# Kernel tuning notes

Measured on AMD Instinct MI355X. Metric: run time of the kernel, lower is better.

## Reference

```python
import jax, jax.numpy as jnp
import numpy as np

D_STATE = 16
D_CONV = 4


def silu(x):
    return x * jax.nn.sigmoid(x)


def selective_scan(x, dt, A, Bm, Cm, Dp):
    # x, dt: (B,L,P); A: (P,N); Bm, Cm: (B,L,N); Dp: (P,)
    dA = jnp.exp(dt[..., None] * A)                    # (B,L,P,N)
    dBx = (dt * x)[..., None] * Bm[:, :, None, :]      # (B,L,P,N)

    def comb(c1, c2):
        a1, b1 = c1
        a2, b2 = c2
        return a1 * a2, a2 * b1 + b2

    _, h = jax.lax.associative_scan(comb, (dA, dBx), axis=1)
    y = jnp.einsum('blpn,bln->blp', h, Cm) + x * Dp
    return y


def mamba(seq, W_in, conv_w, conv_b, W_x, W_dt, b_dt, A_log, Dp, W_out):
    # seq: (B, L, D_model)
    xz = seq @ W_in.T                                  # (B,L,2P)
    P = xz.shape[-1] // 2
    x, z = xz[..., :P], xz[..., P:]
    # causal depthwise conv over L
    xc = jnp.transpose(x, (0, 2, 1))                   # (B,P,L)
    xc = jax.lax.conv_general_dilated(xc, conv_w[:, None, :], (1,),
                                      [(D_CONV - 1, 0)], feature_group_count=P)
    x = silu(jnp.transpose(xc, (0, 2, 1)) + conv_b)    # (B,L,P)
    proj = x @ W_x.T                                   # (B,L, dt_rank+2N)
    dtr = W_dt.shape[1]
    dt = jax.nn.softplus(proj[..., :dtr] @ W_dt.T + b_dt)
    Bm = proj[..., dtr:dtr + D_STATE]
    Cm = proj[..., dtr + D_STATE:]
    A = -jnp.exp(A_log)
    y = selective_scan(x, dt, A, Bm, Cm, Dp)
    y = y * silu(z)
    return y @ W_out.T                                 # (B,L,D_model)


def oss_forward(x1, x2, W_in, conv_w, conv_b, W_x, W_dt, b_dt, A_log, Dp, W_out):
    B, C, H, W = x1.shape
    L = H * W
    seq_h = jnp.transpose(x1.reshape(B, C, L), (0, 2, 1))                       # (B, H*W, C) row-major
    seq_w = jnp.transpose(jnp.transpose(x1, (0, 1, 3, 2)).reshape(B, C, L), (0, 2, 1))  # column-major

    def run(i, s):
        return mamba(s, W_in[i], conv_w[i], conv_b[i], W_x[i], W_dt[i],
                     b_dt[i], A_log[i], Dp[i], W_out[i])

    y_hf = run(0, seq_h)
    y_hb = jnp.flip(run(1, jnp.flip(seq_h, 1)), 1)
    y_wf = run(2, seq_w)
    y_wb = jnp.flip(run(3, jnp.flip(seq_w, 1)), 1)

    y_h = jnp.transpose((y_hf + y_hb).reshape(B, H, W, C), (0, 3, 1, 2))        # (B,C,H,W)
    y_w = jnp.transpose((y_wf + y_wb).reshape(B, W, H, C), (0, 3, 2, 1))        # (B,C,H,W)
    return y_h + y_w + x2


def setup_inputs() -> dict:
    key = jax.random.key(0)
    ks = jax.random.split(key, 12)
    B, C, H, W = 2, 96, 64, 64
    P = 2 * C            # d_inner = expand * d_model = 192
    N = D_STATE
    dtr = -(-C // 16)    # dt_rank = ceil(C/16) = 6
    s = 0.02
    inp = {
        'x1': jax.random.normal(ks[0], (B, C, H, W), jnp.float32),
        'x2': jax.random.normal(ks[1], (B, C, H, W), jnp.float32),
        'W_in': jax.random.normal(ks[2], (4, 2 * P, C), jnp.float32) * s,
        'conv_w': jax.random.normal(ks[3], (4, P, D_CONV), jnp.float32) * s,
        'conv_b': jnp.zeros((4, P), jnp.float32),
        'W_x': jax.random.normal(ks[4], (4, dtr + 2 * N, P), jnp.float32) * s,
        'W_dt': jax.random.normal(ks[5], (4, P, dtr), jnp.float32) * s,
        'b_dt': jax.random.normal(ks[6], (4, P), jnp.float32) * s,
        'A_log': jnp.log(jnp.tile(jnp.arange(1.0, N + 1.0, dtype=jnp.float32), (4, P, 1))),
        'Dp': jnp.ones((4, P), jnp.float32),
        'W_out': jax.random.normal(ks[7], (4, C, P), jnp.float32) * s,
    }
    return inp


def reference(x1, x2, W_in, conv_w, conv_b, W_x, W_dt, b_dt, A_log, Dp, W_out):
    return oss_forward(x1, x2, W_in, conv_w, conv_b, W_x, W_dt, b_dt, A_log, Dp, W_out)
```

## Files before the change

kernel.cpp:

```cpp
#include <hip/hip_runtime.h>

#define D_DIRS 4
#define BB 2
#define CC 96
#define LL 4096
#define PP 192
#define TWOP 384
#define NN 16
#define DTR 6
#define NPROJ 38
#define PROJW 40
#define NCH 256
#define CLEN 16
#define SEQT 24576
#define LOG2E 1.44269504088896340736f

typedef __bf16 bf16x8 __attribute__((ext_vector_type(8)));
typedef float f32x4 __attribute__((ext_vector_type(4)));

__device__ __forceinline__ float fast_softplus(float v) {
    return fmaxf(v, 0.0f) + __logf(1.0f + __expf(-fabsf(v)));
}

__device__ __forceinline__ const float* uptr(const float* p) {
    unsigned long v = (unsigned long)p;
    unsigned lo = __builtin_amdgcn_readfirstlane((unsigned)v);
    unsigned hi = __builtin_amdgcn_readfirstlane((unsigned)(v >> 32));
    return (const float*)(((unsigned long)hi << 32) | (unsigned long)lo);
}

__device__ __constant__ float LOGN[16] = {
    0.0f, 0.6931471806f, 1.0986122887f, 1.3862943611f,
    1.6094379124f, 1.7917594692f, 1.9459101091f, 2.0794415417f,
    2.1972245773f, 2.3025850930f, 2.3978952728f, 2.4849066498f,
    2.5649493575f, 2.6390573296f, 2.7080502011f, 2.7725887222f };

#define POWERS(e1, E)                                                    \
    float E##2 = (e1)*(e1), E##4 = E##2*E##2, E##8 = E##4*E##4;          \
    float E##3 = E##2*(e1), E##5 = E##4*(e1), E##6 = E##4*E##2,          \
          E##7 = E##4*E##3, E##9 = E##8*(e1), E##10 = E##8*E##2,         \
          E##11 = E##8*E##3, E##12 = E##8*E##4, E##13 = E##8*E##5,       \
          E##14 = E##8*E##6, E##15 = E##8*E##7, E##16 = E##8*E##8;

__global__ __launch_bounds__(256) void k_setup(
    const float* __restrict__ W_in, const float* __restrict__ W_x,
    const float* __restrict__ W_out, const float* __restrict__ x1,
    __bf16* __restrict__ wbin, __bf16* __restrict__ wbx, __bf16* __restrict__ wbout,
    __bf16* __restrict__ imgH, __bf16* __restrict__ imgW)
{
    __shared__ float t[96 * 65];
    const int tid = threadIdx.x;
    if (blockIdx.x < 1074) {
        int i = blockIdx.x * 256 + tid;
        const int n0 = 4 * 384 * 104, n1 = 4 * 48 * 200, n2 = 4 * 96 * 200;
        if (i < n0) {
            int c = i % 104, jd = i / 104;
            wbin[i] = (c < 96) ? (__bf16)W_in[jd * 96 + c] : (__bf16)0.0f;
        } else if (i < n0 + n1) {
            int k = i - n0;
            int c = k % 200, jd = k / 200;
            int d = jd / 48, j = jd - d * 48;
            float v = (j < 38 && c < 192) ? W_x[(d * 38 + j) * 192 + c] : 0.0f;
            wbx[k] = (__bf16)v;
        } else if (i < n0 + n1 + n2) {
            int k = i - n0 - n1;
            int c = k % 200, jd = k / 200;
            float v = (c < 192) ? W_out[jd * 192 + c] : 0.0f;
            wbout[k] = (__bf16)v;
        }
    } else {
        const int bx = blockIdx.x - 1074;
        const int b = bx >> 6;
        const int lt = bx & 63;
        for (int i = tid; i < 96 * 64; i += 256) {
            int c = i >> 6, lw = i & 63;
            t[c * 65 + lw] = x1[((b * 96 + c) << 12) + (lt << 6) + lw];
        }
        __syncthreads();
        for (int i = tid; i < 64 * 12; i += 256) {
            int lw = i / 12, q = i - lw * 12;
            union { __bf16 h[8]; uint4 u; } pk;
#pragma unroll
            for (int j = 0; j < 8; ++j) pk.h[j] = (__bf16)t[(q * 8 + j) * 65 + lw];
            ((uint4*)(imgH + (long)((b << 12) + (lt << 6) + lw) * 104))[q] = pk.u;
            ((uint4*)(imgW + (long)((b << 12) + (lw << 6) + lt) * 104))[q] = pk.u;
        }
    }
}

__global__ __launch_bounds__(256) void k_gemm_in(
    const __bf16* __restrict__ imgH, const __bf16* __restrict__ imgW,
    const __bf16* __restrict__ wbin, __bf16* __restrict__ xzb, __bf16* __restrict__ zb)
{
    __shared__ __align__(16) __bf16 As[64 * 104];
    __shared__ __align__(16) __bf16 Bs[128 * 104];
    const int db = blockIdx.y;
    const int d = db >> 1, b = db & 1;
    const int t0 = blockIdx.x * 64;
    const int tid = threadIdx.x;
    const __bf16* img = (d < 2 ? imgH : imgW) + (long)b * (LL * 104);

    {
        uint4* adst = (uint4*)As;
        for (int i = tid; i < 832; i += 256) {
            int r = i / 13, q = i - r * 13;
            int l = (d & 1) ? (LL - 1 - (t0 + r)) : (t0 + r);
            adst[i] = ((const uint4*)(img + (long)l * 104))[q];
        }
    }

    const int lane = tid & 63;
    const int w = tid >> 6;
    const int wm = (w >> 1) * 32, wn = (w & 1) * 32;
    const int lr = lane & 15, lk = (lane >> 4) * 8;
    const int orow = (lane >> 4) * 4;

    for (int jo = 0; jo < TWOP; jo += 128) {
        __syncthreads();
        {
            const uint4* bsrc = (const uint4*)(wbin + (long)(d * TWOP + jo) * 104);
            uint4* bdst = (uint4*)Bs;
            for (int i = tid; i < 1664; i += 256) bdst[i] = bsrc[i];
        }
        __syncthreads();

#pragma unroll
        for (int half = 0; half < 2; ++half) {
            const int j0 = jo + half * 64;
            const __bf16* Bh = Bs + half * (64 * 104);
            f32x4 acc[2][2] = {{{0.f,0.f,0.f,0.f},{0.f,0.f,0.f,0.f}},
                               {{0.f,0.f,0.f,0.f},{0.f,0.f,0.f,0.f}}};
#pragma unroll
            for (int ks = 0; ks < 96; ks += 32) {
                bf16x8 a0 = *(const bf16x8*)&As[(wm + lr) * 104 + ks + lk];
                bf16x8 a1 = *(const bf16x8*)&As[(wm + 16 + lr) * 104 + ks + lk];
                bf16x8 b0 = *(const bf16x8*)&Bh[(wn + lr) * 104 + ks + lk];
                bf16x8 b1 = *(const bf16x8*)&Bh[(wn + 16 + lr) * 104 + ks + lk];
                acc[0][0] = __builtin_amdgcn_mfma_f32_16x16x32_bf16(a0, b0, acc[0][0], 0, 0, 0);
                acc[0][1] = __builtin_amdgcn_mfma_f32_16x16x32_bf16(a0, b1, acc[0][1], 0, 0, 0);
                acc[1][0] = __builtin_amdgcn_mfma_f32_16x16x32_bf16(a1, b0, acc[1][0], 0, 0, 0);
                acc[1][1] = __builtin_amdgcn_mfma_f32_16x16x32_bf16(a1, b1, acc[1][1], 0, 0, 0);
            }
#pragma unroll
            for (int mi = 0; mi < 2; ++mi)
#pragma unroll
                for (int ni = 0; ni < 2; ++ni) {
                    long mbase = (long)(db * LL + t0 + wm + mi * 16 + orow);
                    int jcol = j0 + wn + ni * 16 + lr;
                    if (j0 < PP) {
#pragma unroll
                        for (int r = 0; r < 4; ++r) xzb[(mbase + r) * PP + jcol] = (__bf16)acc[mi][ni][r];
                    } else {
#pragma unroll
                        for (int r = 0; r < 4; ++r) zb[(mbase + r) * PP + jcol - PP] = (__bf16)acc[mi][ni][r];
                    }
                }
        }
    }
}

__global__ __launch_bounds__(256) void k_convproj(
    const __bf16* __restrict__ xzb, const float* __restrict__ conv_w,
    const float* __restrict__ conv_b, const __bf16* __restrict__ wbx,
    __bf16* __restrict__ xb16, float* __restrict__ proj)
{
    __shared__ __align__(16) __bf16 As[64 * 200];
    __shared__ __align__(16) __bf16 Bs[48 * 200];
    const int db = blockIdx.y;
    const int d = db >> 1;
    const int t0 = blockIdx.x * 64;
    const int m0 = db * LL + t0;
    const int tid = threadIdx.x;

    if (tid < 192) {
        const int p = tid;
        const float* wp = conv_w + (d * PP + p) * 4;
        float w0 = wp[0], w1 = wp[1], w2 = wp[2], w3 = wp[3];
        float bias = conv_b[d * PP + p];
        const __bf16* xcol = xzb + (long)m0 * PP + p;
        float x0, x1, x2;
        if (t0 == 0) { x0 = 0.f; x1 = 0.f; x2 = 0.f; }
        else { x0 = (float)xcol[-3 * PP]; x1 = (float)xcol[-2 * PP]; x2 = (float)xcol[-PP]; }
#pragma unroll 8
        for (int t = 0; t < 64; ++t) {
            float x3 = (float)xcol[t * PP];
            float acc = bias + w0 * x0 + w1 * x1 + w2 * x2 + w3 * x3;
            float s = acc / (1.0f + __expf(-acc));
            __bf16 sb = (__bf16)s;
            As[t * 200 + p] = sb;
            xb16[(long)(m0 + t) * 200 + p] = sb;
            x0 = x1; x1 = x2; x2 = x3;
        }
    } else {
        const uint4* bsrc = (const uint4*)(wbx + (long)d * 48 * 200);
        uint4* bdst = (uint4*)Bs;
        for (int i = tid - 192; i < 1200; i += 64) bdst[i] = bsrc[i];
    }
    __syncthreads();

    const int lane = tid & 63;
    const int w = tid >> 6;
    const int lr = lane & 15, lk = (lane >> 4) * 8;
    const int orow = (lane >> 4) * 4;

    f32x4 acc[3] = {{0.f,0.f,0.f,0.f},{0.f,0.f,0.f,0.f},{0.f,0.f,0.f,0.f}};
#pragma unroll
    for (int ks = 0; ks < 192; ks += 32) {
        bf16x8 a = *(const bf16x8*)&As[(w * 16 + lr) * 200 + ks + lk];
#pragma unroll
        for (int ni = 0; ni < 3; ++ni) {
            bf16x8 bfr = *(const bf16x8*)&Bs[(ni * 16 + lr) * 200 + ks + lk];
            acc[ni] = __builtin_amdgcn_mfma_f32_16x16x32_bf16(a, bfr, acc[ni], 0, 0, 0);
        }
    }
#pragma unroll
    for (int ni = 0; ni < 3; ++ni) {
        int j = ni * 16 + lr;
        if (j < NPROJ) {
            int col = (j < 6) ? j : j + 2;
#pragma unroll
            for (int r = 0; r < 4; ++r) {
                int m = m0 + w * 16 + orow + r;
                proj[(long)m * PROJW + col] = acc[ni][r];
            }
        }
    }
}

__global__ __launch_bounds__(256) void k_gemm_out(
    const __bf16* __restrict__ ysb, const __bf16* __restrict__ wbout, float* __restrict__ yo)
{
    __shared__ __align__(16) __bf16 As[64 * 200];
    __shared__ __align__(16) __bf16 Bs[96 * 200];
    const int m0 = blockIdx.x * 64;
    const int d = m0 >> 13;
    const int tid = threadIdx.x;

    for (int i = tid; i < 1600; i += 256) {
        int r = i / 25, q = i - r * 25;
        ((uint4*)As)[i] = ((const uint4*)(ysb + (long)(m0 + r) * 200))[q];
    }
    {
        const uint4* bsrc = (const uint4*)(wbout + (long)d * 96 * 200);
        uint4* bdst = (uint4*)Bs;
        for (int i = tid; i < 2400; i += 256) bdst[i] = bsrc[i];
    }
    __syncthreads();

    const int lane = tid & 63;
    const int w = tid >> 6;
    const int wm = (w >> 1) * 32, wn = (w & 1) * 48;
    const int lr = lane & 15, lk = (lane >> 4) * 8;
    const int orow = (lane >> 4) * 4;

    f32x4 acc[2][3] = {};
#pragma unroll
    for (int ks = 0; ks < 192; ks += 32) {
        bf16x8 a0 = *(const bf16x8*)&As[(wm + lr) * 200 + ks + lk];
        bf16x8 a1 = *(const bf16x8*)&As[(wm + 16 + lr) * 200 + ks + lk];
#pragma unroll
        for (int ni = 0; ni < 3; ++ni) {
            bf16x8 bfr = *(const bf16x8*)&Bs[(wn + ni * 16 + lr) * 200 + ks + lk];
            acc[0][ni] = __builtin_amdgcn_mfma_f32_16x16x32_bf16(a0, bfr, acc[0][ni], 0, 0, 0);
            acc[1][ni] = __builtin_amdgcn_mfma_f32_16x16x32_bf16(a1, bfr, acc[1][ni], 0, 0, 0);
        }
    }
#pragma unroll
    for (int mi = 0; mi < 2; ++mi)
#pragma unroll
        for (int ni = 0; ni < 3; ++ni) {
#pragma unroll
            for (int r = 0; r < 4; ++r) {
                int m = m0 + wm + mi * 16 + orow + r;
                yo[(long)m * CC + wn + ni * 16 + lr] = acc[mi][ni][r];
            }
        }
}

__global__ __launch_bounds__(192) void k_pass1(
    const __bf16* __restrict__ xb16, const float* __restrict__ proj,
    const float* __restrict__ A_log, const float* __restrict__ W_dt,
    const float* __restrict__ b_dt,
    float* __restrict__ sdt_buf, float* __restrict__ cb_pa, float* __restrict__ cb_h)
{
    const int p = threadIdx.x;
    const int chunk = blockIdx.x;
    const int db = blockIdx.y;
    const int d = db >> 1;
    const int m0 = db * LL + chunk * CLEN;

    bool fastA = true;
    float A2[16];
    {
        const float* al = A_log + (d * PP + p) * NN;
#pragma unroll
        for (int n = 0; n < 16; ++n) {
            float av = al[n];
            fastA = fastA && (fabsf(av - LOGN[n]) < 1e-4f);
            A2[n] = av;
        }
    }
    float w[6];
    const float* wd = W_dt + (d * PP + p) * DTR;
#pragma unroll
    for (int r = 0; r < 6; ++r) w[r] = wd[r];
    const float bdt = b_dt[d * PP + p];
    float h[16];
#pragma unroll
    for (int n = 0; n < 16; ++n) h[n] = 0.f;
    float sdt = 0.f;

    const float* prow = uptr(proj + (long)m0 * PROJW);
    const __bf16* xrow = xb16 + (long)m0 * 200 + p;

    if (fastA) {
#pragma unroll
        for (int s = 0; s < CLEN; ++s) {
            const float* row = prow + s * PROJW;
            float4 d0 = *(const float4*)(row);
            float4 d1 = *(const float4*)(row + 4);
            float v = bdt + d0.x*w[0] + d0.y*w[1] + d0.z*w[2] + d0.w*w[3] + d1.x*w[4] + d1.y*w[5];
            float dtv = fast_softplus(v);
            sdt += dtv;
            float dtx = dtv * (float)xrow[s * 200];
            float e1 = exp2f(-LOG2E * dtv);
            POWERS(e1, e)
            const float4* B4 = (const float4*)(row + 8);
            float4 B0 = B4[0], B1 = B4[1], B2v = B4[2], B3 = B4[3];
            h[0]  = e1 *h[0]  + dtx*B0.x;  h[1]  = e2 *h[1]  + dtx*B0.y;
            h[2]  = e3 *h[2]  + dtx*B0.z;  h[3]  = e4 *h[3]  + dtx*B0.w;
            h[4]  = e5 *h[4]  + dtx*B1.x;  h[5]  = e6 *h[5]  + dtx*B1.y;
            h[6]  = e7 *h[6]  + dtx*B1.z;  h[7]  = e8 *h[7]  + dtx*B1.w;
            h[8]  = e9 *h[8]  + dtx*B2v.x; h[9]  = e10*h[9]  + dtx*B2v.y;
            h[10] = e11*h[10] + dtx*B2v.z; h[11] = e12*h[11] + dtx*B2v.w;
            h[12] = e13*h[12] + dtx*B3.x;  h[13] = e14*h[13] + dtx*B3.y;
            h[14] = e15*h[14] + dtx*B3.z;  h[15] = e16*h[15] + dtx*B3.w;
        }
        const long cbase = (long)chunk * SEQT + db * PP + p;
        sdt_buf[chunk * 1536 + db * PP + p] = sdt;
#pragma unroll
        for (int n = 0; n < 16; ++n) cb_h[cbase + n * 1536] = h[n];
    } else {
#pragma unroll
        for (int n = 0; n < 16; ++n) A2[n] = -__expf(A2[n]) * LOG2E;
        for (int s = 0; s < CLEN; ++s) {
            const float* row = prow + s * PROJW;
            float4 d0 = *(const float4*)(row);
            float4 d1 = *(const float4*)(row + 4);
            float v = bdt + d0.x*w[0] + d0.y*w[1] + d0.z*w[2] + d0.w*w[3] + d1.x*w[4] + d1.y*w[5];
            float dtv = fast_softplus(v);
            sdt += dtv;
            float dtx = dtv * (float)xrow[s * 200];
            const float* B = row + 8;
#pragma unroll
            for (int n = 0; n < 16; ++n)
                h[n] = exp2f(dtv * A2[n]) * h[n] + dtx * B[n];
        }
        const long cbase = (long)chunk * SEQT + db * PP + p;
#pragma unroll
        for (int n = 0; n < 16; ++n) {
            cb_pa[cbase + n * 1536] = exp2f(A2[n] * sdt);
            cb_h [cbase + n * 1536] = h[n];
        }
    }
}

__global__ void k_chunkscan(const float* __restrict__ A_log, const float* __restrict__ sdt,
                            const float* __restrict__ cb_pa, float* __restrict__ cb_h)
{
    int j = blockIdx.x * 256 + threadIdx.x;
    int n = j / 1536;
    int r = j - n * 1536;
    int d = r / 384;
    int p = r % PP;

    bool fastA = true;
    const float* al = A_log + (d * PP + p) * NN;
#pragma unroll
    for (int k = 0; k < 16; ++k) fastA = fastA && (fabsf(al[k] - LOGN[k]) < 1e-4f);

    float run = 0.0f;
    if (fastA) {
        const float scale = -LOG2E * (float)(n + 1);
        for (int c = 0; c < NCH; c += 8) {
            float sv[8], hh[8];
#pragma unroll
            for (int i = 0; i < 8; ++i) {
                sv[i] = sdt[(c + i) * 1536 + r];
                hh[i] = cb_h[(long)(c + i) * SEQT + j];
            }
#pragma unroll
            for (int i = 0; i < 8; ++i) {
                cb_h[(long)(c + i) * SEQT + j] = run;
                run = exp2f(scale * sv[i]) * run + hh[i];
            }
        }
    } else {
        for (int c = 0; c < NCH; c += 8) {
            float pa[8], hh[8];
#pragma unroll
            for (int i = 0; i < 8; ++i) {
                long o = (long)(c + i) * SEQT + j;
                pa[i] = cb_pa[o]; hh[i] = cb_h[o];
            }
#pragma unroll
            for (int i = 0; i < 8; ++i) {
                cb_h[(long)(c + i) * SEQT + j] = run;
                run = pa[i] * run + hh[i];
            }
        }
    }
}

__global__ __launch_bounds__(192) void k_pass2(
    const __bf16* __restrict__ xb16, const float* __restrict__ proj,
    const float* __restrict__ A_log, const float* __restrict__ W_dt,
    const float* __restrict__ b_dt, const float* __restrict__ Dp,
    const __bf16* __restrict__ zb, const float* __restrict__ cb_h,
    __bf16* __restrict__ ysb)
{
    const int p = threadIdx.x;
    const int chunk = blockIdx.x;
    const int db = blockIdx.y;
    const int d = db >> 1;
    const int m0 = db * LL + chunk * CLEN;

    bool fastA = true;
    float A2[16];
    {
        const float* al = A_log + (d * PP + p) * NN;
#pragma unroll
        for (int n = 0; n < 16; ++n) {
            float av = al[n];
            fastA = fastA && (fabsf(av - LOGN[n]) < 1e-4f);
            A2[n] = av;
        }
    }
    float w[6];
    const float* wd = W_dt + (d * PP + p) * DTR;
#pragma unroll
    for (int r = 0; r < 6; ++r) w[r] = wd[r];
    const float bdt = b_dt[d * PP + p];
    const float Dv = Dp[d * PP + p];

    float h[16];
    const long cbase = (long)chunk * SEQT + db * PP + p;
#pragma unroll
    for (int n = 0; n < 16; ++n) h[n] = cb_h[cbase + n * 1536];

    const float* prow = uptr(proj + (long)m0 * PROJW);
    const __bf16* xrow = xb16 + (long)m0 * 200 + p;
    const __bf16* zrow = zb + (long)m0 * PP + p;
    __bf16* yrow = ysb + (long)m0 * 200 + p;

    if (fastA) {
#pragma unroll
        for (int s = 0; s < CLEN; ++s) {
            const float* row = prow + s * PROJW;
            float4 d0 = *(const float4*)(row);
            float4 d1 = *(const float4*)(row + 4);
            float v = bdt + d0.x*w[0] + d0.y*w[1] + d0.z*w[2] + d0.w*w[3] + d1.x*w[4] + d1.y*w[5];
            float dtv = fast_softplus(v);
            float xvv = (float)xrow[s * 200];
            float dtx = dtv * xvv;
            float e1 = exp2f(-LOG2E * dtv);
            POWERS(e1, e)
            const float4* B4 = (const float4*)(row + 8);
            const float4* C4 = (const float4*)(row + 24);
            float4 B0 = B4[0], B1 = B4[1], B2v = B4[2], B3 = B4[3];
            float4 C0 = C4[0], C1 = C4[1], C2v = C4[2], C3 = C4[3];
            float y = 0.f;
            h[0]  = e1 *h[0]  + dtx*B0.x;  y += h[0] *C0.x;
            h[1]  = e2 *h[1]  + dtx*B0.y;  y += h[1] *C0.y;
            h[2]  = e3 *h[2]  + dtx*B0.z;  y += h[2] *C0.z;
            h[3]  = e4 *h[3]  + dtx*B0.w;  y += h[3] *C0.w;
            h[4]  = e5 *h[4]  + dtx*B1.x;  y += h[4] *C1.x;
            h[5]  = e6 *h[5]  + dtx*B1.y;  y += h[5] *C1.y;
            h[6]  = e7 *h[6]  + dtx*B1.z;  y += h[6] *C1.z;
            h[7]  = e8 *h[7]  + dtx*B1.w;  y += h[7] *C1.w;
            h[8]  = e9 *h[8]  + dtx*B2v.x; y += h[8] *C2v.x;
            h[9]  = e10*h[9]  + dtx*B2v.y; y += h[9] *C2v.y;
            h[10] = e11*h[10] + dtx*B2v.z; y += h[10]*C2v.z;
            h[11] = e12*h[11] + dtx*B2v.w; y += h[11]*C2v.w;
            h[12] = e13*h[12] + dtx*B3.x;  y += h[12]*C3.x;
            h[13] = e14*h[13] + dtx*B3.y;  y += h[13]*C3.y;
            h[14] = e15*h[14] + dtx*B3.z;  y += h[14]*C3.z;
            h[15] = e16*h[15] + dtx*B3.w;  y += h[15]*C3.w;
            float zvv = (float)zrow[s * PP];
            yrow[s * 200] = (__bf16)((y + xvv * Dv) * (zvv / (1.0f + __expf(-zvv))));
        }
    } else {
#pragma unroll
        for (int n = 0; n < 16; ++n) A2[n] = -__expf(A2[n]) * LOG2E;
        for (int s = 0; s < CLEN; ++s) {
            const float* row = prow + s * PROJW;
            float4 d0 = *(const float4*)(row);
            float4 d1 = *(const float4*)(row + 4);
            float v = bdt + d0.x*w[0] + d0.y*w[1] + d0.z*w[2] + d0.w*w[3] + d1.x*w[4] + d1.y*w[5];
            float dtv = fast_softplus(v);
            float xvv = (float)xrow[s * 200];
            float dtx = dtv * xvv;
            const float* B = row + 8;
            const float* C = row + 24;
            float y = 0.f;
#pragma unroll
            for (int n = 0; n < 16; ++n) {
                h[n] = exp2f(dtv * A2[n]) * h[n] + dtx * B[n];
                y += h[n] * C[n];
            }
            float zvv = (float)zrow[s * PP];
            yrow[s * 200] = (__bf16)((y + xvv * Dv) * (zvv / (1.0f + __expf(-zvv))));
        }
    }
}

__global__ void k_final(const float* __restrict__ x2, const float* __restrict__ yo,
                        float* __restrict__ out)
{
    int idx = blockIdx.x * blockDim.x + threadIdx.x;
    const int total = BB * CC * LL;
    for (; idx < total; idx += gridDim.x * blockDim.x) {
        int w = idx & 63;
        int h = (idx >> 6) & 63;
        int c = (idx >> 12) % CC;
        int b = idx / (CC * LL);
        int lh = (h << 6) | w;
        int lw = (w << 6) | h;
        long m0 = (long)(0 * BB + b) * LL + lh;
        long m1 = (long)(1 * BB + b) * LL + (LL - 1 - lh);
        long m2 = (long)(2 * BB + b) * LL + lw;
        long m3 = (long)(3 * BB + b) * LL + (LL - 1 - lw);
        out[idx] = x2[idx] + yo[m0 * CC + c] + yo[m1 * CC + c] + yo[m2 * CC + c] + yo[m3 * CC + c];
    }
}

extern "C" void kernel_launch(void* const* d_in, const int* in_sizes, int n_in,
                              void* d_out, int out_size, void* d_ws, size_t ws_size,
                              hipStream_t stream)
{
    const float* x1     = (const float*)d_in[0];
    const float* x2     = (const float*)d_in[1];
    const float* W_in   = (const float*)d_in[2];
    const float* conv_w = (const float*)d_in[3];
    const float* conv_b = (const float*)d_in[4];
    const float* W_x    = (const float*)d_in[5];
    const float* W_dt   = (const float*)d_in[6];
    const float* b_dt   = (const float*)d_in[7];
    const float* A_log  = (const float*)d_in[8];
    const float* Dp     = (const float*)d_in[9];
    const float* W_out  = (const float*)d_in[10];
    float* out = (float*)d_out;
    float* ws  = (float*)d_ws;

    __bf16* xzb   = (__bf16*)ws;
    __bf16* zb    = (__bf16*)(ws + 6291456);
    __bf16* xb16  = (__bf16*)(ws + 9437184);
    float*  proj  = ws + 12713984;
    float*  cb_pa = ws + 14024704;
    float*  cb_h  = ws + 20316160;
    __bf16* imgH  = (__bf16*)(ws + 26607616);
    __bf16* imgW  = (__bf16*)(ws + 27033600);
    __bf16* wbin  = (__bf16*)(ws + 27459584);
    __bf16* wbx   = (__bf16*)(ws + 27539456);
    __bf16* wbout = (__bf16*)(ws + 27558656);
    float*  sdt   = ws + 27597056;
    __bf16* ysb = (__bf16*)ws;
    float*  yo  = cb_pa;

    k_setup<<<dim3(1202), 256, 0, stream>>>(W_in, W_x, W_out, x1, wbin, wbx, wbout, imgH, imgW);
    k_gemm_in<<<dim3(64, 8), 256, 0, stream>>>(imgH, imgW, wbin, xzb, zb);
    k_convproj<<<dim3(64, 8), 256, 0, stream>>>(xzb, conv_w, conv_b, wbx, xb16, proj);
    k_pass1<<<dim3(NCH, 8), 192, 0, stream>>>(xb16, proj, A_log, W_dt, b_dt, sdt, cb_pa, cb_h);
    k_chunkscan<<<dim3(SEQT / 256), 256, 0, stream>>>(A_log, sdt, cb_pa, cb_h);
    k_pass2<<<dim3(NCH, 8), 192, 0, stream>>>(xb16, proj, A_log, W_dt, b_dt, Dp, zb, cb_h, ysb);
    k_gemm_out<<<dim3(512), 256, 0, stream>>>(ysb, wbout, yo);
    k_final<<<dim3(3072), 256, 0, stream>>>(x2, yo, out);
}
```

Baseline: 153.2 us.

## Fuse scan pass2 with output projection GEMM through shared memory

Merges the second scan pass and the output-projection MFMA GEMM into one kernel. Each 768-thread block runs four 16-step chunks, writes the gated y tile (64 rows) into LDS, then multiplies it by W_out held in LDS. This removes the ysb global round-trip and one kernel launch. It also drops the readfirstlane scalarisation of the proj pointer, and the larger blocks and LDS use (about 64KB) may lower occupancy, while each block reloads W_out.

```diff
diff --git a/kernel.cpp b/kernel.cpp
--- a/kernel.cpp
+++ b/kernel.cpp
@@ -20,13 +20,6 @@
 
 __device__ __forceinline__ float fast_softplus(float v) {
     return fmaxf(v, 0.0f) + __logf(1.0f + __expf(-fabsf(v)));
-}
-
-__device__ __forceinline__ const float* uptr(const float* p) {
-    unsigned long v = (unsigned long)p;
-    unsigned lo = __builtin_amdgcn_readfirstlane((unsigned)v);
-    unsigned hi = __builtin_amdgcn_readfirstlane((unsigned)(v >> 32));
-    return (const float*)(((unsigned long)hi << 32) | (unsigned long)lo);
 }
 
 __device__ __constant__ float LOGN[16] = {
@@ -227,56 +220,6 @@
     }
 }
 
-__global__ __launch_bounds__(256) void k_gemm_out(
-    const __bf16* __restrict__ ysb, const __bf16* __restrict__ wbout, float* __restrict__ yo)
-{
-    __shared__ __align__(16) __bf16 As[64 * 200];
-    __shared__ __align__(16) __bf16 Bs[96 * 200];
-    const int m0 = blockIdx.x * 64;
-    const int d = m0 >> 13;
-    const int tid = threadIdx.x;
-
-    for (int i = tid; i < 1600; i += 256) {
-        int r = i / 25, q = i - r * 25;
-        ((uint4*)As)[i] = ((const uint4*)(ysb + (long)(m0 + r) * 200))[q];
-    }
-    {
-        const uint4* bsrc = (const uint4*)(wbout + (long)d * 96 * 200);
-        uint4* bdst = (uint4*)Bs;
-        for (int i = tid; i < 2400; i += 256) bdst[i] = bsrc[i];
-    }
-    __syncthreads();
-
-    const int lane = tid & 63;
-    const int w = tid >> 6;
-    const int wm = (w >> 1) * 32, wn = (w & 1) * 48;
-    const int lr = lane & 15, lk = (lane >> 4) * 8;
-    const int orow = (lane >> 4) * 4;
-
-    f32x4 acc[2][3] = {};
-#pragma unroll
-    for (int ks = 0; ks < 192; ks += 32) {
-        bf16x8 a0 = *(const bf16x8*)&As[(wm + lr) * 200 + ks + lk];
-        bf16x8 a1 = *(const bf16x8*)&As[(wm + 16 + lr) * 200 + ks + lk];
-#pragma unroll
-        for (int ni = 0; ni < 3; ++ni) {
-            bf16x8 bfr = *(const bf16x8*)&Bs[(wn + ni * 16 + lr) * 200 + ks + lk];
-            acc[0][ni] = __builtin_amdgcn_mfma_f32_16x16x32_bf16(a0, bfr, acc[0][ni], 0, 0, 0);
-            acc[1][ni] = __builtin_amdgcn_mfma_f32_16x16x32_bf16(a1, bfr, acc[1][ni], 0, 0, 0);
-        }
-    }
-#pragma unroll
-    for (int mi = 0; mi < 2; ++mi)
-#pragma unroll
-        for (int ni = 0; ni < 3; ++ni) {
-#pragma unroll
-            for (int r = 0; r < 4; ++r) {
-                int m = m0 + wm + mi * 16 + orow + r;
-                yo[(long)m * CC + wn + ni * 16 + lr] = acc[mi][ni][r];
-            }
-        }
-}
-
 __global__ __launch_bounds__(192) void k_pass1(
     const __bf16* __restrict__ xb16, const float* __restrict__ proj,
     const float* __restrict__ A_log, const float* __restrict__ W_dt,
@@ -310,7 +253,7 @@
     for (int n = 0; n < 16; ++n) h[n] = 0.f;
     float sdt = 0.f;
 
-    const float* prow = uptr(proj + (long)m0 * PROJW);
+    const float* prow = proj + (long)m0 * PROJW;
     const __bf16* xrow = xb16 + (long)m0 * 200 + p;
 
     if (fastA) {
@@ -412,18 +355,30 @@
     }
 }
 
-__global__ __launch_bounds__(192) void k_pass2(
+__global__ __launch_bounds__(768) void k_pass2out(
     const __bf16* __restrict__ xb16, const float* __restrict__ proj,
     const float* __restrict__ A_log, const float* __restrict__ W_dt,
     const float* __restrict__ b_dt, const float* __restrict__ Dp,
     const __bf16* __restrict__ zb, const float* __restrict__ cb_h,
-    __bf16* __restrict__ ysb)
-{
-    const int p = threadIdx.x;
-    const int chunk = blockIdx.x;
+    const __bf16* __restrict__ wbout, float* __restrict__ yo)
+{
+    __shared__ __align__(16) __bf16 ysl[64 * 200];
+    __shared__ __align__(16) __bf16 Bs[96 * 200];
+    const int tid = threadIdx.x;
+    const int blk = blockIdx.x;
     const int db = blockIdx.y;
     const int d = db >> 1;
+    const int sub = tid / 192;
+    const int p = tid - sub * 192;
+    const int chunk = blk * 4 + sub;
     const int m0 = db * LL + chunk * CLEN;
+    const int m0blk = db * LL + blk * 64;
+
+    {
+        const uint4* bsrc = (const uint4*)(wbout + (long)d * 96 * 200);
+        uint4* bdst = (uint4*)Bs;
+        for (int i = tid; i < 2400; i += 768) bdst[i] = bsrc[i];
+    }
 
     bool fastA = true;
     float A2[16];
@@ -448,10 +403,10 @@
 #pragma unroll
     for (int n = 0; n < 16; ++n) h[n] = cb_h[cbase + n * 1536];
 
-    const float* prow = uptr(proj + (long)m0 * PROJW);
+    const float* prow = proj + (long)m0 * PROJW;
     const __bf16* xrow = xb16 + (long)m0 * 200 + p;
     const __bf16* zrow = zb + (long)m0 * PP + p;
-    __bf16* yrow = ysb + (long)m0 * 200 + p;
+    __bf16* yout = ysl + (sub * CLEN) * 200 + p;
 
     if (fastA) {
 #pragma unroll
@@ -487,7 +442,7 @@
             h[14] = e15*h[14] + dtx*B3.z;  y += h[14]*C3.z;
             h[15] = e16*h[15] + dtx*B3.w;  y += h[15]*C3.w;
             float zvv = (float)zrow[s * PP];
-            yrow[s * 200] = (__bf16)((y + xvv * Dv) * (zvv / (1.0f + __expf(-zvv))));
+            yout[s * 200] = (__bf16)((y + xvv * Dv) * (zvv / (1.0f + __expf(-zvv))));
         }
     } else {
 #pragma unroll
@@ -509,7 +464,30 @@
                 y += h[n] * C[n];
             }
             float zvv = (float)zrow[s * PP];
-            yrow[s * 200] = (__bf16)((y + xvv * Dv) * (zvv / (1.0f + __expf(-zvv))));
+            yout[s * 200] = (__bf16)((y + xvv * Dv) * (zvv / (1.0f + __expf(-zvv))));
+        }
+    }
+    __syncthreads();
+
+    const int lane = tid & 63;
+    const int wv = tid >> 6;
+    const int lr = lane & 15, lk = (lane >> 4) * 8;
+    const int orow = (lane >> 4) * 4;
+#pragma unroll
+    for (int it = 0; it < 2; ++it) {
+        int t = wv * 2 + it;
+        int mi = t & 3, ci = t >> 2;
+        f32x4 acc = {0.f, 0.f, 0.f, 0.f};
+#pragma unroll
+        for (int ks = 0; ks < 192; ks += 32) {
+            bf16x8 a = *(const bf16x8*)&ysl[(mi * 16 + lr) * 200 + ks + lk];
+            bf16x8 bfr = *(const bf16x8*)&Bs[(ci * 16 + lr) * 200 + ks + lk];
+            acc = __builtin_amdgcn_mfma_f32_16x16x32_bf16(a, bfr, acc, 0, 0, 0);
+        }
+#pragma unroll
+        for (int r = 0; r < 4; ++r) {
+            int m = m0blk + mi * 16 + orow + r;
+            yo[(long)m * CC + ci * 16 + lr] = acc[r];
         }
     }
 }
@@ -564,7 +542,6 @@
     __bf16* wbx   = (__bf16*)(ws + 27539456);
     __bf16* wbout = (__bf16*)(ws + 27558656);
     float*  sdt   = ws + 27597056;
-    __bf16* ysb = (__bf16*)ws;
     float*  yo  = cb_pa;
 
     k_setup<<<dim3(1202), 256, 0, stream>>>(W_in, W_x, W_out, x1, wbin, wbx, wbout, imgH, imgW);
@@ -572,7 +549,6 @@
     k_convproj<<<dim3(64, 8), 256, 0, stream>>>(xzb, conv_w, conv_b, wbx, xb16, proj);
     k_pass1<<<dim3(NCH, 8), 192, 0, stream>>>(xb16, proj, A_log, W_dt, b_dt, sdt, cb_pa, cb_h);
     k_chunkscan<<<dim3(SEQT / 256), 256, 0, stream>>>(A_log, sdt, cb_pa, cb_h);
-    k_pass2<<<dim3(NCH, 8), 192, 0, stream>>>(xb16, proj, A_log, W_dt, b_dt, Dp, zb, cb_h, ysb);
-    k_gemm_out<<<dim3(512), 256, 0, stream>>>(ysb, wbout, yo);
+    k_pass2out<<<dim3(64, 8), 768, 0, stream>>>(xb16, proj, A_log, W_dt, b_dt, Dp, zb, cb_h, wbout, yo);
     k_final<<<dim3(3072), 256, 0, stream>>>(x2, yo, out);
 }
```

Result: faster. 136.2 us (-11.1%).
